# Kernel tuning notes

Measured on AMD Instinct MI355X. Metric: run time of the kernel, lower is better.

## Reference

```python
import jax, jax.numpy as jnp
import numpy as np

WH, WW = 8, 8
DIM, HEADS = 512, 16
HEAD_DIM = DIM // HEADS
SCALE = HEAD_DIM ** (-0.5)


def _rel_pos_index(wh, ww):
    # Swin relative position index, computed once with numpy (static).
    coords = np.stack(np.meshgrid(np.arange(wh), np.arange(ww), indexing='ij'))  # [2,wh,ww]
    cf = coords.reshape(2, -1)                                # [2, N]
    rel = cf[:, :, None] - cf[:, None, :]                     # [2, N, N]
    rel = rel.transpose(1, 2, 0).astype(np.int64)             # [N, N, 2]
    rel[..., 0] += wh - 1
    rel[..., 1] += ww - 1
    rel[..., 0] *= 2 * ww - 1
    return jnp.asarray(rel.sum(-1))                           # [N, N]

REL_IDX = _rel_pos_index(WH, WW)


def setup_inputs() -> dict:
    key = jax.random.key(0)
    ks = jax.random.split(key, 12)
    B_, N, C = 1024, WH * WW, DIM
    nW = 64
    std = C ** (-0.5)
    return {
        'q': jax.random.normal(ks[0], (B_, N, C), jnp.float32),
        'k': jax.random.normal(ks[1], (B_, N, C), jnp.float32),
        'v': jax.random.normal(ks[2], (B_, N, C), jnp.float32),
        'mask': jnp.zeros((nW, N, N), jnp.float32),
        'Wq': jax.random.normal(ks[3], (C, C), jnp.float32) * std,
        'bq': jnp.zeros((C,), jnp.float32),
        'Wk': jax.random.normal(ks[4], (C, C), jnp.float32) * std,
        'bk': jnp.zeros((C,), jnp.float32),
        'Wv': jax.random.normal(ks[5], (C, C), jnp.float32) * std,
        'bv': jnp.zeros((C,), jnp.float32),
        'Wp': jax.random.normal(ks[6], (C, C), jnp.float32) * std,
        'bp': jnp.zeros((C,), jnp.float32),
        'bias_table': jax.random.normal(ks[7], ((2 * WH - 1) * (2 * WW - 1), HEADS), jnp.float32) * 0.02,
    }


def reference(q, k, v, mask, Wq, bq, Wk, bk, Wv, bv, Wp, bp, bias_table):
    B_, N, C = q.shape
    H, hd = HEADS, HEAD_DIM

    def heads(x, W, b):  # Linear then split heads -> [B_, H, N, hd]
        return (x @ W.T + b).reshape(B_, N, H, hd).transpose(0, 2, 1, 3)

    qh = heads(q, Wq, bq) * SCALE
    kh = heads(k, Wk, bk)
    vh = heads(v, Wv, bv)

    attn = jnp.einsum('bhnd,bhmd->bhnm', qh, kh)              # [B_, H, N, N]
    rel_bias = bias_table[REL_IDX.reshape(-1)].reshape(N, N, H).transpose(2, 0, 1)  # [H,N,N]
    attn = attn + rel_bias[None]

    nW = mask.shape[0]
    attn = attn.reshape(B_ // nW, nW, H, N, N) + mask[None, :, None]
    attn = attn.reshape(B_, H, N, N)
    attn = jax.nn.softmax(attn, axis=-1)

    x = jnp.einsum('bhnm,bhmd->bhnd', attn, vh)
    x = x.transpose(0, 2, 1, 3).reshape(B_, N, C)
    return x @ Wp.T + bp
```

## Files before the change

kernel.cpp:

```cpp
#include <hip/hip_runtime.h>
#include <hip/hip_bf16.h>

typedef __attribute__((ext_vector_type(4))) float  f32x4;
typedef __attribute__((ext_vector_type(8))) short  bf16x8;
typedef __attribute__((ext_vector_type(4))) short  short4_t;
typedef unsigned short u16;

#define SCALE_Q 0.17677669529663687f

__device__ __forceinline__ short bfc(float f) {
    __bf16 b = (__bf16)f;
    union { __bf16 b; short s; } u; u.b = b; return u.s;
}

__device__ __forceinline__ bf16x8 pack8(f32x4 a, f32x4 b) {
    bf16x8 o;
    o[0] = bfc(a[0]); o[1] = bfc(a[1]); o[2] = bfc(a[2]); o[3] = bfc(a[3]);
    o[4] = bfc(b[0]); o[5] = bfc(b[1]); o[6] = bfc(b[2]); o[7] = bfc(b[3]);
    return o;
}

__device__ __forceinline__ void load_lds16(const void* g, void* l) {
    __builtin_amdgcn_global_load_lds(
        (const __attribute__((address_space(1))) void*)g,
        (__attribute__((address_space(3))) void*)l, 16, 0, 0);
}

__global__ __launch_bounds__(256) void cvt_kernel(
        const float* __restrict__ s, u16* __restrict__ d, int n8)
{
    const int i = blockIdx.x * 256 + threadIdx.x;
    if (i >= n8) return;
    const float4* sp = (const float4*)s + (size_t)i * 2;
    const float4 a = sp[0], b = sp[1];
    bf16x8 o;
    o[0] = bfc(a.x); o[1] = bfc(a.y); o[2] = bfc(a.z); o[3] = bfc(a.w);
    o[4] = bfc(b.x); o[5] = bfc(b.y); o[6] = bfc(b.z); o[7] = bfc(b.w);
    *((bf16x8*)d + i) = o;
}

__global__ __launch_bounds__(256) void cwb_kernel(
        const float* __restrict__ bias_table,
        const float* __restrict__ mask,
        float* __restrict__ cwb)
{
    const int wh = blockIdx.x;
    const int w = wh >> 4, h = wh & 15;
    for (int e = threadIdx.x; e < 4096; e += 256) {
        const int i = e >> 6, j = e & 63;
        const int rel = ((i >> 3) - (j >> 3) + 7) * 15 + (i & 7) - (j & 7) + 7;
        cwb[(size_t)wh * 4096 + e] = bias_table[rel * 16 + h] + mask[(size_t)w * 4096 + e];
    }
}

template<int AFP32, int OMODE>
__global__ __launch_bounds__(256) void gemm_k(
        const void* __restrict__ Aptr, const u16* __restrict__ Wb,
        const float* __restrict__ bias, float scale, void* __restrict__ outp)
{
    __shared__ __align__(16) unsigned char Asb[AFP32 ? 32768 : 16384];
    __shared__ __align__(16) u16 Bs[8192];

    const int wg = (blockIdx.x & 7) * 256 + (blockIdx.x >> 3);
    const int m0 = (wg >> 2) << 7;
    const int n0 = (wg & 3) << 7;

    const int t = threadIdx.x;
    const int lane = t & 63, wv = t >> 6;
    const int g = lane >> 4, ln = lane & 15;
    const int wr = wv >> 1, wc = wv & 1;

    f32x4 acc[4][4];
#pragma unroll
    for (int i = 0; i < 4; i++)
#pragma unroll
        for (int j = 0; j < 4; j++) acc[i][j] = {0.f, 0.f, 0.f, 0.f};

    for (int k0 = 0; k0 < 512; k0 += 64) {
        if (AFP32) {
            const float* Ab = (const float*)Aptr + (size_t)m0 * 512;
#pragma unroll
            for (int c = 0; c < 8; c++) {
                const int bi  = (c << 8) + (wv << 6) + lane;
                const int row = bi >> 4;
                const int col = ((bi & 15) ^ (row & 7)) << 2;
                load_lds16(Ab + (size_t)row * 512 + k0 + col,
                           &Asb[((c << 8) + (wv << 6)) << 4]);
            }
        } else {
            const u16* Ab = (const u16*)Aptr + (size_t)m0 * 512;
#pragma unroll
            for (int c = 0; c < 4; c++) {
                const int bi  = (c << 8) + (wv << 6) + lane;
                const int row = bi >> 3;
                const int col = ((bi & 7) ^ (row & 7)) << 3;
                load_lds16(Ab + (size_t)row * 512 + k0 + col,
                           &Asb[((c << 8) + (wv << 6)) << 4]);
            }
        }
        {
            const u16* Bb = Wb + (size_t)n0 * 512;
#pragma unroll
            for (int c = 0; c < 4; c++) {
                const int bi  = (c << 8) + (wv << 6) + lane;
                const int row = bi >> 3;
                const int col = ((bi & 7) ^ (row & 7)) << 3;
                load_lds16(Bb + (size_t)row * 512 + k0 + col,
                           &Bs[((c << 8) + (wv << 6)) << 3]);
            }
        }
        __syncthreads();

#pragma unroll
        for (int ks = 0; ks < 2; ks++) {
            bf16x8 af[4], bfr[4];
#pragma unroll
            for (int mt = 0; mt < 4; mt++) {
                const int row = (wr << 6) + (mt << 4) + ln;
                if (AFP32) {
                    const int lb = (ks << 3) + (g << 1);
                    const f32x4 lo = *(const f32x4*)&Asb[row * 256 + (((lb    ) ^ (row & 7)) << 4)];
                    const f32x4 hi = *(const f32x4*)&Asb[row * 256 + (((lb + 1) ^ (row & 7)) << 4)];
                    af[mt] = pack8(lo, hi);
                } else {
                    af[mt] = *(const bf16x8*)&Asb[(row << 7) + ((((ks << 2) + g) ^ (row & 7)) << 4)];
                }
            }
#pragma unroll
            for (int nt = 0; nt < 4; nt++) {
                const int row = (wc << 6) + (nt << 4) + ln;
                bfr[nt] = *(const bf16x8*)&Bs[(row << 6) + ((((ks << 2) + g) ^ (row & 7)) << 3)];
            }
#pragma unroll
            for (int mt = 0; mt < 4; mt++)
#pragma unroll
                for (int nt = 0; nt < 4; nt++)
                    acc[mt][nt] = __builtin_amdgcn_mfma_f32_16x16x32_bf16(
                        af[mt], bfr[nt], acc[mt][nt], 0, 0, 0);
        }
        __syncthreads();
    }

#pragma unroll
    for (int mt = 0; mt < 4; mt++) {
#pragma unroll
        for (int nt = 0; nt < 4; nt++) {
            const int n = n0 + (wc << 6) + (nt << 4) + ln;
            const float bv = bias[n];
            const int mbase = m0 + (wr << 6) + (mt << 4) + (g << 2);
            if (OMODE == 0) {
#pragma unroll
                for (int r = 0; r < 4; r++) {
                    const int m = mbase + r;
                    const int b = m >> 6, tt = m & 63, hh = n >> 5, d = n & 31;
                    ((u16*)outp)[((size_t)(b * 16 + hh) * 64 + tt) * 32 + d] =
                        (u16)bfc((acc[mt][nt][r] + bv) * scale);
                }
            } else if (OMODE == 1) {
                short4_t hq;
#pragma unroll
                for (int r = 0; r < 4; r++) hq[r] = bfc((acc[mt][nt][r] + bv) * scale);
                const int b = mbase >> 6, tt = mbase & 63, hh = n >> 5, d = n & 31;
                *(short4_t*)&((u16*)outp)[((size_t)(b * 16 + hh) * 32 + d) * 64 + tt] = hq;
            } else {
#pragma unroll
                for (int r = 0; r < 4; r++) {
                    const int m = mbase + r;
                    ((float*)outp)[(size_t)m * 512 + n] = (acc[mt][nt][r] + bv) * scale;
                }
            }
        }
    }
}

__global__ __launch_bounds__(256) void attn_kernel(
        const u16* __restrict__ qh, const u16* __restrict__ kh,
        const u16* __restrict__ vt, const float* __restrict__ cwb,
        u16* __restrict__ xout)
{
    __shared__ __align__(16) u16 P[16384];

    const int wv = threadIdx.x >> 6;
    const int bid = (blockIdx.x << 2) + wv;
    const int b = bid >> 4, h = bid & 15, w = b & 63;
    const int lane = threadIdx.x & 63, g = lane >> 4, ln = lane & 15;
    const size_t base = (size_t)bid * 2048;
    u16* Pw = &P[wv << 12];

    bf16x8 kf[4], qf[4];
#pragma unroll
    for (int mt = 0; mt < 4; mt++)
        kf[mt] = *(const bf16x8*)&kh[base + (mt * 16 + ln) * 32 + g * 8];
#pragma unroll
    for (int nt = 0; nt < 4; nt++)
        qf[nt] = *(const bf16x8*)&qh[base + (nt * 16 + ln) * 32 + g * 8];

    f32x4 acc[4][4];
#pragma unroll
    for (int i = 0; i < 4; i++)
#pragma unroll
        for (int j = 0; j < 4; j++) acc[i][j] = {0.f, 0.f, 0.f, 0.f};

#pragma unroll
    for (int mt = 0; mt < 4; mt++)
#pragma unroll
        for (int nt = 0; nt < 4; nt++)
            acc[mt][nt] = __builtin_amdgcn_mfma_f32_16x16x32_bf16(
                kf[mt], qf[nt], acc[mt][nt], 0, 0, 0);

    const float* cw = cwb + (size_t)(w * 16 + h) * 4096;
#pragma unroll
    for (int nt = 0; nt < 4; nt++) {
        const int i = nt * 16 + ln;
#pragma unroll
        for (int mt = 0; mt < 4; mt++) {
            const float4 bm = *(const float4*)&cw[i * 64 + mt * 16 + (g << 2)];
            acc[mt][nt][0] += bm.x; acc[mt][nt][1] += bm.y;
            acc[mt][nt][2] += bm.z; acc[mt][nt][3] += bm.w;
        }
    }

#pragma unroll
    for (int nt = 0; nt < 4; nt++) {
        float mx = acc[0][nt][0];
#pragma unroll
        for (int mt = 0; mt < 4; mt++)
#pragma unroll
            for (int r = 0; r < 4; r++) mx = fmaxf(mx, acc[mt][nt][r]);
        mx = fmaxf(mx, __shfl_xor(mx, 16));
        mx = fmaxf(mx, __shfl_xor(mx, 32));
        float sum = 0.f;
#pragma unroll
        for (int mt = 0; mt < 4; mt++)
#pragma unroll
            for (int r = 0; r < 4; r++) {
                const float p = __expf(acc[mt][nt][r] - mx);
                acc[mt][nt][r] = p;
                sum += p;
            }
        sum += __shfl_xor(sum, 16);
        sum += __shfl_xor(sum, 32);
        const float rs = 1.0f / sum;
        const int i = nt * 16 + ln;
#pragma unroll
        for (int mt = 0; mt < 4; mt++) {
            short4_t hq;
#pragma unroll
            for (int r = 0; r < 4; r++) hq[r] = bfc(acc[mt][nt][r] * rs);
            const int idx = (i * 64 + mt * 16 + (g << 2)) ^ ((i & 7) << 3);
            *(short4_t*)&Pw[idx] = hq;
        }
    }
    __syncthreads();

    f32x4 oacc[2][4];
#pragma unroll
    for (int i = 0; i < 2; i++)
#pragma unroll
        for (int j = 0; j < 4; j++) oacc[i][j] = {0.f, 0.f, 0.f, 0.f};

#pragma unroll
    for (int ks = 0; ks < 2; ks++) {
        bf16x8 vf[2], pf[4];
#pragma unroll
        for (int mt = 0; mt < 2; mt++)
            vf[mt] = *(const bf16x8*)&vt[base + (mt * 16 + ln) * 64 + ks * 32 + g * 8];
#pragma unroll
        for (int nt = 0; nt < 4; nt++) {
            const int i = nt * 16 + ln;
            pf[nt] = *(const bf16x8*)&Pw[(i * 64 + ks * 32 + g * 8) ^ ((i & 7) << 3)];
        }
#pragma unroll
        for (int mt = 0; mt < 2; mt++)
#pragma unroll
            for (int nt = 0; nt < 4; nt++)
                oacc[mt][nt] = __builtin_amdgcn_mfma_f32_16x16x32_bf16(
                    vf[mt], pf[nt], oacc[mt][nt], 0, 0, 0);
    }

#pragma unroll
    for (int mt = 0; mt < 2; mt++) {
#pragma unroll
        for (int nt = 0; nt < 4; nt++) {
            const int i = nt * 16 + ln, d0 = mt * 16 + (g << 2);
            short4_t hq;
#pragma unroll
            for (int r = 0; r < 4; r++) hq[r] = bfc(oacc[mt][nt][r]);
            *(short4_t*)&xout[((size_t)b * 64 + i) * 512 + h * 32 + d0] = hq;
        }
    }
}

extern "C" void kernel_launch(void* const* d_in, const int* in_sizes, int n_in,
                              void* d_out, int out_size, void* d_ws, size_t ws_size,
                              hipStream_t stream) {
    const float* q    = (const float*)d_in[0];
    const float* k    = (const float*)d_in[1];
    const float* v    = (const float*)d_in[2];
    const float* mask = (const float*)d_in[3];
    const float* Wq   = (const float*)d_in[4];
    const float* bq   = (const float*)d_in[5];
    const float* Wk   = (const float*)d_in[6];
    const float* bk   = (const float*)d_in[7];
    const float* Wv   = (const float*)d_in[8];
    const float* bv   = (const float*)d_in[9];
    const float* Wp   = (const float*)d_in[10];
    const float* bp   = (const float*)d_in[11];
    const float* bias_table = (const float*)d_in[12];
    float* out = (float*)d_out;

    char* ws = (char*)d_ws;
    u16*   t0  = (u16*)(ws);
    u16*   qh  = (u16*)(ws + 67108864);
    u16*   kh  = (u16*)(ws + 134217728);
    u16*   vt  = (u16*)(ws + 201326592);
    float* cwb = (float*)(ws + 268435456);
    u16*   wqb = (u16*)(ws + 285212672);
    u16*   wkb = (u16*)(ws + 285736960);
    u16*   wvb = (u16*)(ws + 286261248);
    u16*   wpb = (u16*)(ws + 286785536);

    const int n8_w = (512 * 512) / 8;

    cwb_kernel<<<1024, 256, 0, stream>>>(bias_table, mask, cwb);
    cvt_kernel<<<n8_w / 256, 256, 0, stream>>>(Wq, wqb, n8_w);
    cvt_kernel<<<n8_w / 256, 256, 0, stream>>>(Wk, wkb, n8_w);
    cvt_kernel<<<n8_w / 256, 256, 0, stream>>>(Wv, wvb, n8_w);
    cvt_kernel<<<n8_w / 256, 256, 0, stream>>>(Wp, wpb, n8_w);

    gemm_k<1, 0><<<2048, 256, 0, stream>>>((const void*)q, wqb, bq, SCALE_Q, (void*)qh);
    gemm_k<1, 0><<<2048, 256, 0, stream>>>((const void*)k, wkb, bk, 1.0f,    (void*)kh);
    gemm_k<1, 1><<<2048, 256, 0, stream>>>((const void*)v, wvb, bv, 1.0f,    (void*)vt);

    attn_kernel<<<4096, 256, 0, stream>>>(qh, kh, vt, cwb, t0);

    gemm_k<0, 2><<<2048, 256, 0, stream>>>((const void*)t0, wpb, bp, 1.0f, (void*)out);
}
```

Before: 417.7 us.

## Replace LDS-tiled GEMM with per-wave register-streamed GEMM without shared memory

The projection GEMMs drop LDS staging and block-level barriers. Each wave now computes an independent 64x64 output tile, loading A and B fragments directly from global memory into registers with a two-stage software double buffer. This removes the LDS round trip and the __syncthreads, but loses the operand sharing across the four waves of a block. Global and L2 traffic per output therefore rises, and the per-lane reads become strided across rows.

Result: slower. 893.2 us (+113.8%).

```diff
diff --git a/kernel.cpp b/kernel.cpp
--- a/kernel.cpp
+++ b/kernel.cpp
@@ -18,12 +18,6 @@
     o[0] = bfc(a[0]); o[1] = bfc(a[1]); o[2] = bfc(a[2]); o[3] = bfc(a[3]);
     o[4] = bfc(b[0]); o[5] = bfc(b[1]); o[6] = bfc(b[2]); o[7] = bfc(b[3]);
     return o;
-}
-
-__device__ __forceinline__ void load_lds16(const void* g, void* l) {
-    __builtin_amdgcn_global_load_lds(
-        (const __attribute__((address_space(1))) void*)g,
-        (__attribute__((address_space(3))) void*)l, 16, 0, 0);
 }
 
 __global__ __launch_bounds__(256) void cvt_kernel(
@@ -54,21 +48,17 @@
 }
 
 template<int AFP32, int OMODE>
-__global__ __launch_bounds__(256) void gemm_k(
+__global__ __launch_bounds__(256) void gemm_stream(
         const void* __restrict__ Aptr, const u16* __restrict__ Wb,
         const float* __restrict__ bias, float scale, void* __restrict__ outp)
 {
-    __shared__ __align__(16) unsigned char Asb[AFP32 ? 32768 : 16384];
-    __shared__ __align__(16) u16 Bs[8192];
-
-    const int wg = (blockIdx.x & 7) * 256 + (blockIdx.x >> 3);
-    const int m0 = (wg >> 2) << 7;
-    const int n0 = (wg & 3) << 7;
-
-    const int t = threadIdx.x;
-    const int lane = t & 63, wv = t >> 6;
+    const int bidx = (blockIdx.x & 7) * 256 + (blockIdx.x >> 3);
+    const int wv = threadIdx.x >> 6, lane = threadIdx.x & 63;
     const int g = lane >> 4, ln = lane & 15;
-    const int wr = wv >> 1, wc = wv & 1;
+    const int wt = bidx * 4 + wv;
+    const int m0 = (wt >> 3) << 6;
+    const int n0 = (wt & 7) << 6;
+    const int ko = g << 3;
 
     f32x4 acc[4][4];
 #pragma unroll
@@ -76,78 +66,94 @@
 #pragma unroll
         for (int j = 0; j < 4; j++) acc[i][j] = {0.f, 0.f, 0.f, 0.f};
 
-    for (int k0 = 0; k0 < 512; k0 += 64) {
-        if (AFP32) {
-            const float* Ab = (const float*)Aptr + (size_t)m0 * 512;
-#pragma unroll
-            for (int c = 0; c < 8; c++) {
-                const int bi  = (c << 8) + (wv << 6) + lane;
-                const int row = bi >> 4;
-                const int col = ((bi & 15) ^ (row & 7)) << 2;
-                load_lds16(Ab + (size_t)row * 512 + k0 + col,
-                           &Asb[((c << 8) + (wv << 6)) << 4]);
-            }
-        } else {
-            const u16* Ab = (const u16*)Aptr + (size_t)m0 * 512;
-#pragma unroll
-            for (int c = 0; c < 4; c++) {
-                const int bi  = (c << 8) + (wv << 6) + lane;
-                const int row = bi >> 3;
-                const int col = ((bi & 7) ^ (row & 7)) << 3;
-                load_lds16(Ab + (size_t)row * 512 + k0 + col,
-                           &Asb[((c << 8) + (wv << 6)) << 4]);
-            }
-        }
-        {
-            const u16* Bb = Wb + (size_t)n0 * 512;
-#pragma unroll
-            for (int c = 0; c < 4; c++) {
-                const int bi  = (c << 8) + (wv << 6) + lane;
-                const int row = bi >> 3;
-                const int col = ((bi & 7) ^ (row & 7)) << 3;
-                load_lds16(Bb + (size_t)row * 512 + k0 + col,
-                           &Bs[((c << 8) + (wv << 6)) << 3]);
-            }
-        }
-        __syncthreads();
-
-#pragma unroll
-        for (int ks = 0; ks < 2; ks++) {
-            bf16x8 af[4], bfr[4];
-#pragma unroll
-            for (int mt = 0; mt < 4; mt++) {
-                const int row = (wr << 6) + (mt << 4) + ln;
-                if (AFP32) {
-                    const int lb = (ks << 3) + (g << 1);
-                    const f32x4 lo = *(const f32x4*)&Asb[row * 256 + (((lb    ) ^ (row & 7)) << 4)];
-                    const f32x4 hi = *(const f32x4*)&Asb[row * 256 + (((lb + 1) ^ (row & 7)) << 4)];
-                    af[mt] = pack8(lo, hi);
-                } else {
-                    af[mt] = *(const bf16x8*)&Asb[(row << 7) + ((((ks << 2) + g) ^ (row & 7)) << 4)];
-                }
-            }
-#pragma unroll
-            for (int nt = 0; nt < 4; nt++) {
-                const int row = (wc << 6) + (nt << 4) + ln;
-                bfr[nt] = *(const bf16x8*)&Bs[(row << 6) + ((((ks << 2) + g) ^ (row & 7)) << 3)];
-            }
-#pragma unroll
-            for (int mt = 0; mt < 4; mt++)
-#pragma unroll
-                for (int nt = 0; nt < 4; nt++)
-                    acc[mt][nt] = __builtin_amdgcn_mfma_f32_16x16x32_bf16(
-                        af[mt], bfr[nt], acc[mt][nt], 0, 0, 0);
-        }
-        __syncthreads();
+    const u16* bpm[4];
+#pragma unroll
+    for (int nt = 0; nt < 4; nt++)
+        bpm[nt] = Wb + (size_t)(n0 + nt * 16 + ln) * 512 + ko;
+
+    if (AFP32) {
+        const float* A = (const float*)Aptr;
+        const float* apm[4];
+#pragma unroll
+        for (int mt = 0; mt < 4; mt++)
+            apm[mt] = A + (size_t)(m0 + mt * 16 + ln) * 512 + ko;
+
+#define LOADF(KS, LO, HI, BF) do {                                          \
+    _Pragma("unroll")                                                       \
+    for (int mt = 0; mt < 4; mt++) {                                        \
+        LO[mt] = *(const f32x4*)(apm[mt] + (KS) * 32);                      \
+        HI[mt] = *(const f32x4*)(apm[mt] + (KS) * 32 + 4);                  \
+    }                                                                       \
+    _Pragma("unroll")                                                       \
+    for (int nt = 0; nt < 4; nt++)                                          \
+        BF[nt] = *(const bf16x8*)(bpm[nt] + (KS) * 32);                     \
+} while (0)
+
+#define COMPF(LO, HI, BF) do {                                              \
+    bf16x8 aw_[4];                                                          \
+    _Pragma("unroll")                                                       \
+    for (int mt = 0; mt < 4; mt++) aw_[mt] = pack8(LO[mt], HI[mt]);         \
+    _Pragma("unroll")                                                       \
+    for (int mt = 0; mt < 4; mt++)                                          \
+        _Pragma("unroll")                                                   \
+        for (int nt = 0; nt < 4; nt++)                                      \
+            acc[mt][nt] = __builtin_amdgcn_mfma_f32_16x16x32_bf16(          \
+                aw_[mt], BF[nt], acc[mt][nt], 0, 0, 0);                     \
+} while (0)
+
+        f32x4 lo0[4], hi0[4], lo1[4], hi1[4];
+        bf16x8 b0[4], b1[4];
+        LOADF(0, lo0, hi0, b0);
+#pragma unroll
+        for (int kp = 0; kp < 8; kp++) {
+            LOADF(2 * kp + 1, lo1, hi1, b1);
+            COMPF(lo0, hi0, b0);
+            if (kp < 7) LOADF(2 * kp + 2, lo0, hi0, b0);
+            COMPF(lo1, hi1, b1);
+        }
+    } else {
+        const u16* A = (const u16*)Aptr;
+        const u16* apm[4];
+#pragma unroll
+        for (int mt = 0; mt < 4; mt++)
+            apm[mt] = A + (size_t)(m0 + mt * 16 + ln) * 512 + ko;
+
+#define LOADB(KS, AB, BF) do {                                              \
+    _Pragma("unroll")                                                       \
+    for (int mt = 0; mt < 4; mt++)                                          \
+        AB[mt] = *(const bf16x8*)(apm[mt] + (KS) * 32);                     \
+    _Pragma("unroll")                                                       \
+    for (int nt = 0; nt < 4; nt++)                                          \
+        BF[nt] = *(const bf16x8*)(bpm[nt] + (KS) * 32);                     \
+} while (0)
+
+#define COMPB(AB, BF) do {                                                  \
+    _Pragma("unroll")                                                       \
+    for (int mt = 0; mt < 4; mt++)                                          \
+        _Pragma("unroll")                                                   \
+        for (int nt = 0; nt < 4; nt++)                                      \
+            acc[mt][nt] = __builtin_amdgcn_mfma_f32_16x16x32_bf16(          \
+                AB[mt], BF[nt], acc[mt][nt], 0, 0, 0);                      \
+} while (0)
+
+        bf16x8 a0[4], a1[4], b0[4], b1[4];
+        LOADB(0, a0, b0);
+#pragma unroll
+        for (int kp = 0; kp < 8; kp++) {
+            LOADB(2 * kp + 1, a1, b1);
+            COMPB(a0, b0);
+            if (kp < 7) LOADB(2 * kp + 2, a0, b0);
+            COMPB(a1, b1);
+        }
     }
 
 #pragma unroll
     for (int mt = 0; mt < 4; mt++) {
 #pragma unroll
         for (int nt = 0; nt < 4; nt++) {
-            const int n = n0 + (wc << 6) + (nt << 4) + ln;
+            const int n = n0 + (nt << 4) + ln;
             const float bv = bias[n];
-            const int mbase = m0 + (wr << 6) + (mt << 4) + (g << 2);
+            const int mbase = m0 + (mt << 4) + (g << 2);
             if (OMODE == 0) {
 #pragma unroll
                 for (int r = 0; r < 4; r++) {
@@ -328,11 +334,11 @@
     cvt_kernel<<<n8_w / 256, 256, 0, stream>>>(Wv, wvb, n8_w);
     cvt_kernel<<<n8_w / 256, 256, 0, stream>>>(Wp, wpb, n8_w);
 
-    gemm_k<1, 0><<<2048, 256, 0, stream>>>((const void*)q, wqb, bq, SCALE_Q, (void*)qh);
-    gemm_k<1, 0><<<2048, 256, 0, stream>>>((const void*)k, wkb, bk, 1.0f,    (void*)kh);
-    gemm_k<1, 1><<<2048, 256, 0, stream>>>((const void*)v, wvb, bv, 1.0f,    (void*)vt);
+    gemm_stream<1, 0><<<2048, 256, 0, stream>>>((const void*)q, wqb, bq, SCALE_Q, (void*)qh);
+    gemm_stream<1, 0><<<2048, 256, 0, stream>>>((const void*)k, wkb, bk, 1.0f,    (void*)kh);
+    gemm_stream<1, 1><<<2048, 256, 0, stream>>>((const void*)v, wvb, bv, 1.0f,    (void*)vt);
 
     attn_kernel<<<4096, 256, 0, stream>>>(qh, kh, vt, cwb, t0);
 
-    gemm_k<0, 2><<<2048, 256, 0, stream>>>((const void*)t0, wpb, bp, 1.0f, (void*)out);
-}
+    gemm_stream<0, 2><<<2048, 256, 0, stream>>>((const void*)t0, wpb, bp, 1.0f, (void*)out);
+}
```

## Use 256x256 double-buffered bf16 GEMM with separate activation conversion

Applied to the files above, without the earlier changes.

Replaces the 128x128 projection GEMM, which loaded fp32 activations and converted them in LDS, with a 256x256-tile, 512-thread GEMM. The new GEMM reads pre-converted bf16 inputs and uses a two-stage LDS double buffer with explicit waitcnt/barrier scheduling and raised priority around MFMA. Activations are converted to bf16 by a separate kernel before each GEMM, and the four weight conversions are merged into one launch. The aim is better data reuse and overlap of loads with MFMA; the trade-off is an extra global write and read of each bf16 activation copy.

Result: slower. 701.4 us (+67.9%).

```diff
diff --git a/kernel.cpp b/kernel.cpp
--- a/kernel.cpp
+++ b/kernel.cpp
@@ -11,13 +11,6 @@
 __device__ __forceinline__ short bfc(float f) {
     __bf16 b = (__bf16)f;
     union { __bf16 b; short s; } u; u.b = b; return u.s;
-}
-
-__device__ __forceinline__ bf16x8 pack8(f32x4 a, f32x4 b) {
-    bf16x8 o;
-    o[0] = bfc(a[0]); o[1] = bfc(a[1]); o[2] = bfc(a[2]); o[3] = bfc(a[3]);
-    o[4] = bfc(b[0]); o[5] = bfc(b[1]); o[6] = bfc(b[2]); o[7] = bfc(b[3]);
-    return o;
 }
 
 __device__ __forceinline__ void load_lds16(const void* g, void* l) {
@@ -39,6 +32,25 @@
     *((bf16x8*)d + i) = o;
 }
 
+__global__ __launch_bounds__(256) void wcvt_kernel(
+        const float* __restrict__ w0, const float* __restrict__ w1,
+        const float* __restrict__ w2, const float* __restrict__ w3,
+        u16* __restrict__ d0, u16* __restrict__ d1,
+        u16* __restrict__ d2, u16* __restrict__ d3)
+{
+    const float* s = (blockIdx.y == 0) ? w0 : (blockIdx.y == 1) ? w1
+                   : (blockIdx.y == 2) ? w2 : w3;
+    u16* d = (blockIdx.y == 0) ? d0 : (blockIdx.y == 1) ? d1
+           : (blockIdx.y == 2) ? d2 : d3;
+    const int i = blockIdx.x * 256 + threadIdx.x;
+    const float4* sp = (const float4*)s + (size_t)i * 2;
+    const float4 a = sp[0], b = sp[1];
+    bf16x8 o;
+    o[0] = bfc(a.x); o[1] = bfc(a.y); o[2] = bfc(a.z); o[3] = bfc(a.w);
+    o[4] = bfc(b.x); o[5] = bfc(b.y); o[6] = bfc(b.z); o[7] = bfc(b.w);
+    *((bf16x8*)d + i) = o;
+}
+
 __global__ __launch_bounds__(256) void cwb_kernel(
         const float* __restrict__ bias_table,
         const float* __restrict__ mask,
@@ -53,101 +65,95 @@
     }
 }
 
-template<int AFP32, int OMODE>
-__global__ __launch_bounds__(256) void gemm_k(
-        const void* __restrict__ Aptr, const u16* __restrict__ Wb,
+template<int OMODE>
+__global__ __launch_bounds__(512, 2) void gemm256(
+        const u16* __restrict__ A, const u16* __restrict__ Wb,
         const float* __restrict__ bias, float scale, void* __restrict__ outp)
 {
-    __shared__ __align__(16) unsigned char Asb[AFP32 ? 32768 : 16384];
-    __shared__ __align__(16) u16 Bs[8192];
-
-    const int wg = (blockIdx.x & 7) * 256 + (blockIdx.x >> 3);
-    const int m0 = (wg >> 2) << 7;
-    const int n0 = (wg & 3) << 7;
+    __shared__ __align__(16) u16 As[2][8192];
+    __shared__ __align__(16) u16 Bs[2][8192];
+
+    const int wg = ((blockIdx.x & 7) << 6) + (blockIdx.x >> 3);
+    const int m0 = (wg >> 1) << 8;
+    const int n0 = (wg & 1) << 8;
 
     const int t = threadIdx.x;
     const int lane = t & 63, wv = t >> 6;
     const int g = lane >> 4, ln = lane & 15;
-    const int wr = wv >> 1, wc = wv & 1;
-
-    f32x4 acc[4][4];
-#pragma unroll
-    for (int i = 0; i < 4; i++)
+    const int wr = wv >> 2, wc = wv & 3;
+
+    const u16* Ab = A  + (size_t)m0 * 512;
+    const u16* Bb = Wb + (size_t)n0 * 512;
+
+    f32x4 acc[8][4];
+#pragma unroll
+    for (int i = 0; i < 8; i++)
 #pragma unroll
         for (int j = 0; j < 4; j++) acc[i][j] = {0.f, 0.f, 0.f, 0.f};
 
-    for (int k0 = 0; k0 < 512; k0 += 64) {
-        if (AFP32) {
-            const float* Ab = (const float*)Aptr + (size_t)m0 * 512;
-#pragma unroll
-            for (int c = 0; c < 8; c++) {
-                const int bi  = (c << 8) + (wv << 6) + lane;
-                const int row = bi >> 4;
-                const int col = ((bi & 15) ^ (row & 7)) << 2;
-                load_lds16(Ab + (size_t)row * 512 + k0 + col,
-                           &Asb[((c << 8) + (wv << 6)) << 4]);
-            }
-        } else {
-            const u16* Ab = (const u16*)Aptr + (size_t)m0 * 512;
-#pragma unroll
-            for (int c = 0; c < 4; c++) {
-                const int bi  = (c << 8) + (wv << 6) + lane;
-                const int row = bi >> 3;
-                const int col = ((bi & 7) ^ (row & 7)) << 3;
-                load_lds16(Ab + (size_t)row * 512 + k0 + col,
-                           &Asb[((c << 8) + (wv << 6)) << 4]);
-            }
-        }
-        {
-            const u16* Bb = Wb + (size_t)n0 * 512;
-#pragma unroll
-            for (int c = 0; c < 4; c++) {
-                const int bi  = (c << 8) + (wv << 6) + lane;
-                const int row = bi >> 3;
-                const int col = ((bi & 7) ^ (row & 7)) << 3;
-                load_lds16(Bb + (size_t)row * 512 + k0 + col,
-                           &Bs[((c << 8) + (wv << 6)) << 3]);
-            }
-        }
-        __syncthreads();
-
-#pragma unroll
-        for (int ks = 0; ks < 2; ks++) {
-            bf16x8 af[4], bfr[4];
-#pragma unroll
-            for (int mt = 0; mt < 4; mt++) {
-                const int row = (wr << 6) + (mt << 4) + ln;
-                if (AFP32) {
-                    const int lb = (ks << 3) + (g << 1);
-                    const f32x4 lo = *(const f32x4*)&Asb[row * 256 + (((lb    ) ^ (row & 7)) << 4)];
-                    const f32x4 hi = *(const f32x4*)&Asb[row * 256 + (((lb + 1) ^ (row & 7)) << 4)];
-                    af[mt] = pack8(lo, hi);
-                } else {
-                    af[mt] = *(const bf16x8*)&Asb[(row << 7) + ((((ks << 2) + g) ^ (row & 7)) << 4)];
-                }
-            }
-#pragma unroll
-            for (int nt = 0; nt < 4; nt++) {
-                const int row = (wc << 6) + (nt << 4) + ln;
-                bfr[nt] = *(const bf16x8*)&Bs[(row << 6) + ((((ks << 2) + g) ^ (row & 7)) << 3)];
-            }
-#pragma unroll
-            for (int mt = 0; mt < 4; mt++)
-#pragma unroll
-                for (int nt = 0; nt < 4; nt++)
-                    acc[mt][nt] = __builtin_amdgcn_mfma_f32_16x16x32_bf16(
-                        af[mt], bfr[nt], acc[mt][nt], 0, 0, 0);
-        }
-        __syncthreads();
-    }
-
-#pragma unroll
-    for (int mt = 0; mt < 4; mt++) {
+#define STAGE(KT, BUF) do {                                                  \
+    _Pragma("unroll")                                                        \
+    for (int c = 0; c < 2; c++) {                                            \
+        const int bi = (c << 9) + t;                  \
+        const int row = bi >> 2, blk = bi & 3;                               \
+        const int col = ((KT) << 5) + ((blk ^ (row & 3)) << 3);              \
+        load_lds16(Ab + (size_t)row * 512 + col, &As[BUF][bi << 3]);         \
+        load_lds16(Bb + (size_t)row * 512 + col, &Bs[BUF][bi << 3]);         \
+    }                                                                        \
+} while (0)
+
+#define COMPUTE(BUF) do {                                                    \
+    bf16x8 bfr[4];                                                           \
+    _Pragma("unroll")                                                        \
+    for (int nt = 0; nt < 4; nt++) {                                         \
+        const int rn = (wc << 6) + (nt << 4) + ln;                           \
+        bfr[nt] = *(const bf16x8*)&Bs[BUF][(rn << 5) + ((g ^ (rn & 3)) << 3)];\
+    }                                                                        \
+    _Pragma("unroll")                                                        \
+    for (int mh = 0; mh < 2; mh++) {                                         \
+        bf16x8 af[4];                                                        \
+        _Pragma("unroll")                                                    \
+        for (int mt = 0; mt < 4; mt++) {                                     \
+            const int rm = (wr << 7) + (mh << 6) + (mt << 4) + ln;           \
+            af[mt] = *(const bf16x8*)&As[BUF][(rm << 5) + ((g ^ (rm & 3)) << 3)];\
+        }                                                                    \
+        __builtin_amdgcn_s_setprio(1);                                       \
+        _Pragma("unroll")                                                    \
+        for (int mt = 0; mt < 4; mt++)                                       \
+            _Pragma("unroll")                                                \
+            for (int nt = 0; nt < 4; nt++)                                   \
+                acc[(mh << 2) + mt][nt] = __builtin_amdgcn_mfma_f32_16x16x32_bf16(\
+                    af[mt], bfr[nt], acc[(mh << 2) + mt][nt], 0, 0, 0);      \
+        __builtin_amdgcn_s_setprio(0);                                       \
+    }                                                                        \
+} while (0)
+
+    STAGE(0, 0);
+    STAGE(1, 1);
+    asm volatile("s_waitcnt vmcnt(4)" ::: "memory");
+    __builtin_amdgcn_s_barrier();
+
+    for (int kt = 0; kt < 16; ++kt) {
+        const int cur = kt & 1;
+        if (cur == 0) COMPUTE(0); else COMPUTE(1);
+        asm volatile("" ::: "memory");
+        __builtin_amdgcn_s_barrier();
+        if (kt < 14) {
+            if (cur == 0) STAGE(kt + 2, 0); else STAGE(kt + 2, 1);
+            asm volatile("s_waitcnt vmcnt(4)" ::: "memory");
+        } else if (kt == 14) {
+            asm volatile("s_waitcnt vmcnt(0)" ::: "memory");
+        }
+        __builtin_amdgcn_s_barrier();
+    }
+
+#pragma unroll
+    for (int mt = 0; mt < 8; mt++) {
 #pragma unroll
         for (int nt = 0; nt < 4; nt++) {
             const int n = n0 + (wc << 6) + (nt << 4) + ln;
             const float bv = bias[n];
-            const int mbase = m0 + (wr << 6) + (mt << 4) + (g << 2);
+            const int mbase = m0 + (wr << 7) + (mt << 4) + (g << 2);
             if (OMODE == 0) {
 #pragma unroll
                 for (int r = 0; r < 4; r++) {
@@ -171,6 +177,8 @@
             }
         }
     }
+#undef STAGE
+#undef COMPUTE
 }
 
 __global__ __launch_bounds__(256) void attn_kernel(
@@ -320,19 +328,21 @@
     u16*   wvb = (u16*)(ws + 286261248);
     u16*   wpb = (u16*)(ws + 286785536);
 
-    const int n8_w = (512 * 512) / 8;
+    const int n8_act = (1024 * 64 * 512) / 8;
 
     cwb_kernel<<<1024, 256, 0, stream>>>(bias_table, mask, cwb);
-    cvt_kernel<<<n8_w / 256, 256, 0, stream>>>(Wq, wqb, n8_w);
-    cvt_kernel<<<n8_w / 256, 256, 0, stream>>>(Wk, wkb, n8_w);
-    cvt_kernel<<<n8_w / 256, 256, 0, stream>>>(Wv, wvb, n8_w);
-    cvt_kernel<<<n8_w / 256, 256, 0, stream>>>(Wp, wpb, n8_w);
-
-    gemm_k<1, 0><<<2048, 256, 0, stream>>>((const void*)q, wqb, bq, SCALE_Q, (void*)qh);
-    gemm_k<1, 0><<<2048, 256, 0, stream>>>((const void*)k, wkb, bk, 1.0f,    (void*)kh);
-    gemm_k<1, 1><<<2048, 256, 0, stream>>>((const void*)v, wvb, bv, 1.0f,    (void*)vt);
+    wcvt_kernel<<<dim3(128, 4), 256, 0, stream>>>(Wq, Wk, Wv, Wp, wqb, wkb, wvb, wpb);
+
+    cvt_kernel<<<n8_act / 256, 256, 0, stream>>>(q, t0, n8_act);
+    gemm256<0><<<512, 512, 0, stream>>>(t0, wqb, bq, SCALE_Q, (void*)qh);
+
+    cvt_kernel<<<n8_act / 256, 256, 0, stream>>>(k, t0, n8_act);
+    gemm256<0><<<512, 512, 0, stream>>>(t0, wkb, bk, 1.0f, (void*)kh);
+
+    cvt_kernel<<<n8_act / 256, 256, 0, stream>>>(v, t0, n8_act);
+    gemm256<1><<<512, 512, 0, stream>>>(t0, wvb, bv, 1.0f, (void*)vt);
 
     attn_kernel<<<4096, 256, 0, stream>>>(qh, kh, vt, cwb, t0);
 
-    gemm_k<0, 2><<<2048, 256, 0, stream>>>((const void*)t0, wpb, bp, 1.0f, (void*)out);
-}
+    gemm256<2><<<512, 512, 0, stream>>>(t0, wpb, bp, 1.0f, (void*)out);
+}
```
